# Optimization experiments

Measured on AMD Instinct MI355X. Metric: run time of the kernel, lower is better.

## Reference

```python
import jax, jax.numpy as jnp
import numpy as np

N_NODES = 100000
N_EDGES = 1600000
IN_DIM, HID_DIM, OUT_DIM = 512, 128, 64


def gcn_layer(x, rows, cols, vals, W, b):
    # support = x @ W; out[i] = sum_{e: rows[e]==i} vals[e] * support[cols[e]] + b
    support = x @ W                      # [N, d_out]
    msgs = vals[:, None] * support[cols]  # [E, d_out] gather
    agg = jax.ops.segment_sum(msgs, rows, num_segments=N_NODES)  # scatter-add
    return agg + b


def setup_inputs() -> dict:
    key = jax.random.key(0)
    ks = jax.random.split(key, 8)
    x = jax.random.normal(ks[0], (N_NODES, IN_DIM), dtype=jnp.float32)
    edge_rows = jax.random.randint(ks[1], (N_EDGES,), 0, N_NODES, dtype=jnp.int32)
    edge_cols = jax.random.randint(ks[2], (N_EDGES,), 0, N_NODES, dtype=jnp.int32)
    edge_vals = jax.random.uniform(ks[3], (N_EDGES,), dtype=jnp.float32)
    W0 = jax.random.normal(ks[4], (IN_DIM, HID_DIM), dtype=jnp.float32) / np.sqrt(IN_DIM)
    b0 = jnp.zeros((HID_DIM,), dtype=jnp.float32)
    W1 = jax.random.normal(ks[5], (HID_DIM, OUT_DIM), dtype=jnp.float32) / np.sqrt(HID_DIM)
    b1 = jnp.zeros((OUT_DIM,), dtype=jnp.float32)
    return {"x": x, "edge_rows": edge_rows, "edge_cols": edge_cols,
            "edge_vals": edge_vals, "W0": W0, "b0": b0, "W1": W1, "b1": b1}


def reference(x, edge_rows, edge_cols, edge_vals, W0, b0, W1, b1):
    h = gcn_layer(x, edge_rows, edge_cols, edge_vals, W0, b0)  # GCN0
    h = jax.nn.relu(h)                                          # activation0
    # dropout: identity in eval mode
    out = gcn_layer(h, edge_rows, edge_cols, edge_vals, W1, b1)  # GCN1
    return out
```

## Files before the change

### kernel.cpp

```cpp
#include <hip/hip_runtime.h>

#define N_NODES 100000
#define N_EDGES 1600000
#define NBUCK   ((N_NODES + 127) / 128)
#define BCAP    4096

typedef __attribute__((ext_vector_type(8))) short bf16x8;
typedef __attribute__((ext_vector_type(4))) float f32x4;

__device__ __forceinline__ unsigned short f2bf(float f) {
    unsigned int u = __builtin_bit_cast(unsigned int, f);
    u = (u + 0x7FFFu + ((u >> 16) & 1u)) >> 16;
    return (unsigned short)u;
}
__device__ __forceinline__ float bfu2f(unsigned short u) {
    return __builtin_bit_cast(float, (unsigned int)u << 16);
}
__device__ __forceinline__ uint2 packbf4(float4 v) {
    uint2 p;
    p.x = (unsigned int)f2bf(v.x) | ((unsigned int)f2bf(v.y) << 16);
    p.y = (unsigned int)f2bf(v.z) | ((unsigned int)f2bf(v.w) << 16);
    return p;
}

__device__ __forceinline__ void block_barrier() {
    asm volatile("s_waitcnt lgkmcnt(0)" ::: "memory");
    __builtin_amdgcn_sched_barrier(0);
    __builtin_amdgcn_s_barrier();
    __builtin_amdgcn_sched_barrier(0);
}

__global__ __launch_bounds__(256) void prep_kernel(const float* __restrict__ W0,
                                                   const float* __restrict__ W1,
                                                   unsigned short* __restrict__ W0t,
                                                   unsigned short* __restrict__ W1t,
                                                   int* __restrict__ bcursor) {
    const int i = blockIdx.x * 256 + threadIdx.x;
    if (i < 512 * 128) {
        const int k = i / 128, c = i % 128;
        W0t[c * 512 + k] = f2bf(W0[i]);
    }
    const int j = i - 512 * 128;
    if (j >= 0 && j < 128 * 64) {
        const int k = j / 64, c = j % 64;
        W1t[c * 128 + k] = f2bf(W1[j]);
    }
    const int z = i - (512 * 128 + 128 * 64);
    if (z >= 0 && z < NBUCK) bcursor[z] = z * BCAP;
}

__global__ __launch_bounds__(256) void gemm1_kernel(const float* __restrict__ A,
                                                    const unsigned short* __restrict__ Wt,
                                                    unsigned short* __restrict__ C, int N) {
    constexpr int K   = 512;
    constexpr int M   = 128;
    constexpr int LDT = 40;

    __shared__ __align__(16) unsigned short As[2][64 * LDT];
    __shared__ __align__(16) unsigned short Bs[2][M * LDT];

    const int tid  = threadIdx.x;
    const int lane = tid & 63;
    const int wid  = tid >> 6;
    const int wm   = wid >> 1;
    const int wn   = wid & 1;
    const int brow = blockIdx.x * 64;

    const int ar0 = tid >> 3, akq = tid & 7;
    const int ar1 = ar0 + 32;
    const bool v0 = (brow + ar0) < N;
    const bool v1 = (brow + ar1) < N;
    const float* ap0 = A + (size_t)(brow + ar0) * K + akq * 4;
    const float* ap1 = A + (size_t)(brow + ar1) * K + akq * 4;
    const int br0 = tid >> 2, bkq = tid & 3;
    const unsigned short* bp0 = Wt + (size_t)br0 * K + bkq * 8;
    const unsigned short* bp1 = Wt + (size_t)(br0 + 64) * K + bkq * 8;

    float4 A0a, A0b, A1a, A1b, A2a, A2b, A3a, A3b;
    uint4  B0a, B0b, B1a, B1b, B2a, B2b, B3a, B3b;

#define ISSUE(s, t) do {                                                          \
        const int ko = (t) * 32;                                                  \
        A##s##a = v0 ? *reinterpret_cast<const float4*>(ap0 + ko)                 \
                     : make_float4(0.f, 0.f, 0.f, 0.f);                           \
        A##s##b = v1 ? *reinterpret_cast<const float4*>(ap1 + ko)                 \
                     : make_float4(0.f, 0.f, 0.f, 0.f);                           \
        B##s##a = *reinterpret_cast<const uint4*>(bp0 + ko);                      \
        B##s##b = *reinterpret_cast<const uint4*>(bp1 + ko);                      \
    } while (0)

#define WLDS(s, buf) do {                                                         \
        *reinterpret_cast<uint2*>(&As[buf][ar0 * LDT + akq * 4]) = packbf4(A##s##a); \
        *reinterpret_cast<uint2*>(&As[buf][ar1 * LDT + akq * 4]) = packbf4(A##s##b); \
        *reinterpret_cast<uint4*>(&Bs[buf][br0 * LDT + bkq * 8]) = B##s##a;          \
        *reinterpret_cast<uint4*>(&Bs[buf][(br0 + 64) * LDT + bkq * 8]) = B##s##b;   \
    } while (0)

    f32x4 acc[2][4];
#pragma unroll
    for (int m = 0; m < 2; ++m)
#pragma unroll
        for (int n = 0; n < 4; ++n) acc[m][n] = (f32x4){0.f, 0.f, 0.f, 0.f};

    const int afo = (wm * 32 + (lane & 15)) * LDT + (lane >> 4) * 8;
    const int bfo = (wn * 64 + (lane & 15)) * LDT + (lane >> 4) * 8;

    auto step = [&](int buf) {
        bf16x8 af[2], bfr[4];
#pragma unroll
        for (int m = 0; m < 2; ++m)
            af[m] = *reinterpret_cast<const bf16x8*>(&As[buf][afo + m * 16 * LDT]);
#pragma unroll
        for (int n = 0; n < 4; ++n)
            bfr[n] = *reinterpret_cast<const bf16x8*>(&Bs[buf][bfo + n * 16 * LDT]);
#pragma unroll
        for (int m = 0; m < 2; ++m)
#pragma unroll
            for (int n = 0; n < 4; ++n)
                acc[m][n] = __builtin_amdgcn_mfma_f32_16x16x32_bf16(af[m], bfr[n], acc[m][n], 0, 0, 0);
    };

    ISSUE(0, 0); ISSUE(1, 1); ISSUE(2, 2); ISSUE(3, 3);
    WLDS(0, 0);
    block_barrier();

#pragma unroll
    for (int i = 0; i < 4; ++i) {
        const int t = 4 * i;
        if (t + 4 < 16) ISSUE(0, t + 4);
        step(0);
        WLDS(1, 1);
        block_barrier();
        if (t + 5 < 16) ISSUE(1, t + 5);
        step(1);
        WLDS(2, 0);
        block_barrier();
        if (t + 6 < 16) ISSUE(2, t + 6);
        step(0);
        WLDS(3, 1);
        block_barrier();
        if (t + 7 < 16) ISSUE(3, t + 7);
        step(1);
        if (t + 4 < 16) WLDS(0, 0);
        block_barrier();
    }
#undef ISSUE
#undef WLDS

    const int rb = brow + wm * 32 + ((lane >> 4) * 4);
    const int cb = wn * 64 + (lane & 15);
#pragma unroll
    for (int m = 0; m < 2; ++m)
#pragma unroll
        for (int n = 0; n < 4; ++n)
#pragma unroll
            for (int j = 0; j < 4; ++j) {
                const int r = rb + m * 16 + j;
                if (r < N) C[(size_t)r * M + cb + n * 16] = f2bf(acc[m][n][j]);
            }
}

__global__ __launch_bounds__(256) void gemm2_kernel(const unsigned short* __restrict__ Hb,
                                                    const unsigned short* __restrict__ Wt,
                                                    unsigned short* __restrict__ C) {
    const int gw = (blockIdx.x * 256 + threadIdx.x) >> 6;
    if (gw >= N_NODES / 16) return;
    const int lane = threadIdx.x & 63;
    const int rlo = lane & 15, khi = lane >> 4;
    const int rb = gw * 16;

    const unsigned short* wp = Wt + (size_t)rlo * 128 + khi * 8;
    bf16x8 b[4][4];
#pragma unroll
    for (int n = 0; n < 4; ++n)
#pragma unroll
        for (int t = 0; t < 4; ++t)
            b[n][t] = *reinterpret_cast<const bf16x8*>(wp + (size_t)n * 16 * 128 + t * 32);

    f32x4 acc[4];
#pragma unroll
    for (int n = 0; n < 4; ++n) acc[n] = (f32x4){0.f, 0.f, 0.f, 0.f};

    const unsigned short* hp = Hb + (size_t)(rb + rlo) * 128 + khi * 8;
#pragma unroll
    for (int t = 0; t < 4; ++t) {
        const bf16x8 af = *reinterpret_cast<const bf16x8*>(hp + t * 32);
#pragma unroll
        for (int n = 0; n < 4; ++n)
            acc[n] = __builtin_amdgcn_mfma_f32_16x16x32_bf16(af, b[n][t], acc[n], 0, 0, 0);
    }

#pragma unroll
    for (int n = 0; n < 4; ++n)
#pragma unroll
        for (int j = 0; j < 4; ++j)
            C[(size_t)(rb + khi * 4 + j) * 64 + n * 16 + rlo] = f2bf(acc[n][j]);
}

#define SCAT_CH 4096
__global__ __launch_bounds__(256) void scatter_bucket_kernel(const int* __restrict__ rows,
                                                             const int* __restrict__ cols,
                                                             const float* __restrict__ vals,
                                                             int* __restrict__ bcursor,
                                                             int2* __restrict__ tmp) {
    __shared__ int hist[NBUCK];
    const int tid = threadIdx.x;
    const int e0  = blockIdx.x * SCAT_CH;

    for (int b = tid; b < NBUCK; b += 256) hist[b] = 0;
    __syncthreads();

#pragma unroll
    for (int i = 0; i < SCAT_CH / 256; ++i) {
        const int e = e0 + i * 256 + tid;
        if (e < N_EDGES) atomicAdd(&hist[rows[e] >> 7], 1);
    }
    __syncthreads();

    for (int b = tid; b < NBUCK; b += 256) {
        const int hcnt = hist[b];
        hist[b] = (hcnt > 0) ? atomicAdd(&bcursor[b], hcnt) : 0;
    }
    __syncthreads();

#pragma unroll
    for (int i = 0; i < SCAT_CH / 256; ++i) {
        const int e = e0 + i * 256 + tid;
        if (e < N_EDGES) {
            const int r   = rows[e];
            const int pos = atomicAdd(&hist[r >> 7], 1);
            tmp[pos] = make_int2(cols[e] | ((r & 127) << 17), __float_as_int(vals[e]));
        }
    }
}

__global__ __launch_bounds__(256) void bucket_csr_kernel(const int* __restrict__ bcursor,
                                                         const int2* __restrict__ tmp,
                                                         int2* __restrict__ meta,
                                                         int2* __restrict__ row_range) {
    __shared__ int cnt_sh[128];
    __shared__ int startsh[128];
    __shared__ int cur[128];
    const int b   = blockIdx.x;
    const int tid = threadIdx.x;
    const int base = b * BCAP;
    const int cnt  = bcursor[b] - base;

    if (tid < 128) cnt_sh[tid] = 0;
    __syncthreads();

    for (int j = tid; j < cnt; j += 256)
        atomicAdd(&cnt_sh[((unsigned int)tmp[base + j].x) >> 17], 1);
    __syncthreads();

    if (tid == 0) {
        int a = base;
        for (int i = 0; i < 128; ++i) { startsh[i] = a; a += cnt_sh[i]; }
    }
    __syncthreads();

    if (tid < 128) {
        cur[tid] = startsh[tid];
        const int row = (b << 7) + tid;
        if (row < N_NODES)
            row_range[row] = make_int2(startsh[tid], startsh[tid] + cnt_sh[tid]);
    }
    __syncthreads();

    for (int j = tid; j < cnt; j += 256) {
        const int2 w  = tmp[base + j];
        const int  rl = ((unsigned int)w.x) >> 17;
        const int  pos = atomicAdd(&cur[rl], 1);
        meta[pos] = make_int2(w.x & 0x1FFFF, w.y);
    }
}

template<int DIM, bool RELU_BF16_OUT>
__global__ __launch_bounds__(256) void spmm_kernel(const int2* __restrict__ row_range,
                                                   const int2* __restrict__ meta,
                                                   const unsigned short* __restrict__ sup,
                                                   const float* __restrict__ bias,
                                                   void* __restrict__ aggv) {
    const int wv = (blockIdx.x * 256 + threadIdx.x) >> 6;
    if (wv >= N_NODES) return;
    const int lane = threadIdx.x & 63;

    constexpr int GL = DIM / 8;
    constexpr int NG = 64 / GL;
    constexpr int UN = 2;
    const int grp = lane / GL;
    const int sub = lane % GL;

    const int2 rr = row_range[wv];
    const int start = rr.x, end = rr.y;

    float a[8] = {0.f, 0.f, 0.f, 0.f, 0.f, 0.f, 0.f, 0.f};

    int j = start + grp;
    while (j + (UN - 1) * NG < end) {
        int2 e[UN];
#pragma unroll
        for (int u = 0; u < UN; ++u) e[u] = meta[j + u * NG];
        bf16x8 s[UN];
#pragma unroll
        for (int u = 0; u < UN; ++u)
            s[u] = *reinterpret_cast<const bf16x8*>(sup + (size_t)e[u].x * DIM + sub * 8);
#pragma unroll
        for (int u = 0; u < UN; ++u) {
            const float v = __int_as_float(e[u].y);
#pragma unroll
            for (int d = 0; d < 8; ++d)
                a[d] = fmaf(v, bfu2f((unsigned short)s[u][d]), a[d]);
        }
        j += UN * NG;
    }
    for (; j < end; j += NG) {
        const int2 e = meta[j];
        const bf16x8 s = *reinterpret_cast<const bf16x8*>(sup + (size_t)e.x * DIM + sub * 8);
        const float v = __int_as_float(e.y);
#pragma unroll
        for (int d = 0; d < 8; ++d)
            a[d] = fmaf(v, bfu2f((unsigned short)s[d]), a[d]);
    }

#pragma unroll
    for (int d = 0; d < 8; ++d) {
        if (GL == 8) a[d] += __shfl_xor(a[d], 8);
        a[d] += __shfl_xor(a[d], 16);
        a[d] += __shfl_xor(a[d], 32);
    }

    if (lane < GL) {
        const float4 b0 = *reinterpret_cast<const float4*>(bias + sub * 8);
        const float4 b1 = *reinterpret_cast<const float4*>(bias + sub * 8 + 4);
        float o[8];
        o[0] = a[0] + b0.x; o[1] = a[1] + b0.y; o[2] = a[2] + b0.z; o[3] = a[3] + b0.w;
        o[4] = a[4] + b1.x; o[5] = a[5] + b1.y; o[6] = a[6] + b1.z; o[7] = a[7] + b1.w;
        if (RELU_BF16_OUT) {
            unsigned short* h = (unsigned short*)aggv;
            bf16x8 r;
#pragma unroll
            for (int d = 0; d < 8; ++d) r[d] = (short)f2bf(fmaxf(o[d], 0.f));
            *reinterpret_cast<bf16x8*>(h + (size_t)wv * DIM + sub * 8) = r;
        } else {
            float* og = (float*)aggv;
            float* dst = og + (size_t)wv * DIM + sub * 8;
            *reinterpret_cast<float4*>(dst)     = make_float4(o[0], o[1], o[2], o[3]);
            *reinterpret_cast<float4*>(dst + 4) = make_float4(o[4], o[5], o[6], o[7]);
        }
    }
}

extern "C" void kernel_launch(void* const* d_in, const int* in_sizes, int n_in,
                              void* d_out, int out_size, void* d_ws, size_t ws_size,
                              hipStream_t stream) {
    const float* x    = (const float*)d_in[0];
    const int*   rows = (const int*)d_in[1];
    const int*   cols = (const int*)d_in[2];
    const float* vals = (const float*)d_in[3];
    const float* W0   = (const float*)d_in[4];
    const float* b0   = (const float*)d_in[5];
    const float* W1   = (const float*)d_in[6];
    const float* b1   = (const float*)d_in[7];
    float*       out  = (float*)d_out;

    char* p = (char*)d_ws;
    unsigned short* sup0 = (unsigned short*)p;  p += (size_t)N_NODES * 128 * 2;
    unsigned short* h    = (unsigned short*)p;  p += (size_t)N_NODES * 128 * 2;
    unsigned short* sup1 = (unsigned short*)p;  p += (size_t)N_NODES * 64 * 2;
    unsigned short* W0t  = (unsigned short*)p;  p += (size_t)512 * 128 * 2;
    unsigned short* W1t  = (unsigned short*)p;  p += (size_t)128 * 64 * 2;
    int*   bcursor  = (int*)p;                  p += (size_t)((NBUCK + 3) / 4) * 16;
    int2*  row_range= (int2*)p;                 p += (size_t)N_NODES * 8;
    int2*  tmp      = (int2*)p;                 p += (size_t)NBUCK * BCAP * 8;
    int2*  meta     = (int2*)p;                 p += (size_t)NBUCK * BCAP * 8;

    const int prep_blocks = (512 * 128 + 128 * 64 + NBUCK + 255) / 256;
    const int scat_blocks = (N_EDGES + SCAT_CH - 1) / SCAT_CH;
    const int gemm_blocks = (N_NODES + 63) / 64;
    const int gem2_blocks = (N_NODES / 16 + 3) / 4;
    const int spmm_blocks = (N_NODES * 64 + 255) / 256;

    prep_kernel<<<prep_blocks, 256, 0, stream>>>(W0, W1, W0t, W1t, bcursor);

    scatter_bucket_kernel<<<scat_blocks, 256, 0, stream>>>(rows, cols, vals, bcursor, tmp);
    bucket_csr_kernel<<<NBUCK, 256, 0, stream>>>(bcursor, tmp, meta, row_range);

    gemm1_kernel<<<gemm_blocks, 256, 0, stream>>>(x, W0t, sup0, N_NODES);
    spmm_kernel<128, true><<<spmm_blocks, 256, 0, stream>>>(row_range, meta, sup0, b0, h);

    gemm2_kernel<<<gem2_blocks, 256, 0, stream>>>(h, W1t, sup1);
    spmm_kernel<64, false><<<spmm_blocks, 256, 0, stream>>>(row_range, meta, sup1, b1, out);
}
```

Baseline: 249.0 us.

## Stage gemm1 tiles via direct global-to-LDS loads with fp32 A in LDS

After: 274.8 us. 1.1x slower.

```diff
diff --git a/kernel.cpp b/kernel.cpp
--- a/kernel.cpp
+++ b/kernel.cpp
@@ -16,18 +16,19 @@
 __device__ __forceinline__ float bfu2f(unsigned short u) {
     return __builtin_bit_cast(float, (unsigned int)u << 16);
 }
-__device__ __forceinline__ uint2 packbf4(float4 v) {
-    uint2 p;
-    p.x = (unsigned int)f2bf(v.x) | ((unsigned int)f2bf(v.y) << 16);
-    p.y = (unsigned int)f2bf(v.z) | ((unsigned int)f2bf(v.w) << 16);
-    return p;
-}
-
-__device__ __forceinline__ void block_barrier() {
-    asm volatile("s_waitcnt lgkmcnt(0)" ::: "memory");
-    __builtin_amdgcn_sched_barrier(0);
-    __builtin_amdgcn_s_barrier();
-    __builtin_amdgcn_sched_barrier(0);
+__device__ __forceinline__ bf16x8 pack8(float4 a, float4 b) {
+    bf16x8 r;
+    r[0] = (short)f2bf(a.x); r[1] = (short)f2bf(a.y);
+    r[2] = (short)f2bf(a.z); r[3] = (short)f2bf(a.w);
+    r[4] = (short)f2bf(b.x); r[5] = (short)f2bf(b.y);
+    r[6] = (short)f2bf(b.z); r[7] = (short)f2bf(b.w);
+    return r;
+}
+
+__device__ __forceinline__ void gl_lds16(const void* g, void* s) {
+    __builtin_amdgcn_global_load_lds(
+        (const __attribute__((address_space(1))) void*)g,
+        (__attribute__((address_space(3))) void*)s, 16, 0, 0);
 }
 
 __global__ __launch_bounds__(256) void prep_kernel(const float* __restrict__ W0,
@@ -52,49 +53,28 @@
 __global__ __launch_bounds__(256) void gemm1_kernel(const float* __restrict__ A,
                                                     const unsigned short* __restrict__ Wt,
                                                     unsigned short* __restrict__ C, int N) {
-    constexpr int K   = 512;
-    constexpr int M   = 128;
-    constexpr int LDT = 40;
-
-    __shared__ __align__(16) unsigned short As[2][64 * LDT];
-    __shared__ __align__(16) unsigned short Bs[2][M * LDT];
+    __shared__ __align__(16) float4 AsF4[2][8 * 64];
+    __shared__ __align__(16) uint4  Bs4[2][4 * 128];
 
     const int tid  = threadIdx.x;
     const int lane = tid & 63;
-    const int wid  = tid >> 6;
-    const int wm   = wid >> 1;
-    const int wn   = wid & 1;
+    const int w    = tid >> 6;
+    const int wm   = w >> 1;
+    const int wn   = w & 1;
     const int brow = blockIdx.x * 64;
 
-    const int ar0 = tid >> 3, akq = tid & 7;
-    const int ar1 = ar0 + 32;
-    const bool v0 = (brow + ar0) < N;
-    const bool v1 = (brow + ar1) < N;
-    const float* ap0 = A + (size_t)(brow + ar0) * K + akq * 4;
-    const float* ap1 = A + (size_t)(brow + ar1) * K + akq * 4;
-    const int br0 = tid >> 2, bkq = tid & 3;
-    const unsigned short* bp0 = Wt + (size_t)br0 * K + bkq * 8;
-    const unsigned short* bp1 = Wt + (size_t)(br0 + 64) * K + bkq * 8;
-
-    float4 A0a, A0b, A1a, A1b, A2a, A2b, A3a, A3b;
-    uint4  B0a, B0b, B1a, B1b, B2a, B2b, B3a, B3b;
-
-#define ISSUE(s, t) do {                                                          \
-        const int ko = (t) * 32;                                                  \
-        A##s##a = v0 ? *reinterpret_cast<const float4*>(ap0 + ko)                 \
-                     : make_float4(0.f, 0.f, 0.f, 0.f);                           \
-        A##s##b = v1 ? *reinterpret_cast<const float4*>(ap1 + ko)                 \
-                     : make_float4(0.f, 0.f, 0.f, 0.f);                           \
-        B##s##a = *reinterpret_cast<const uint4*>(bp0 + ko);                      \
-        B##s##b = *reinterpret_cast<const uint4*>(bp1 + ko);                      \
-    } while (0)
-
-#define WLDS(s, buf) do {                                                         \
-        *reinterpret_cast<uint2*>(&As[buf][ar0 * LDT + akq * 4]) = packbf4(A##s##a); \
-        *reinterpret_cast<uint2*>(&As[buf][ar1 * LDT + akq * 4]) = packbf4(A##s##b); \
-        *reinterpret_cast<uint4*>(&Bs[buf][br0 * LDT + bkq * 8]) = B##s##a;          \
-        *reinterpret_cast<uint4*>(&Bs[buf][(br0 + 64) * LDT + bkq * 8]) = B##s##b;   \
-    } while (0)
+    const int grow = min(brow + lane, N - 1);
+    const float* asrc = A + (size_t)grow * 512;
+    const unsigned short* bsrc0 = Wt + (size_t)(lane)      * 512 + w * 8;
+    const unsigned short* bsrc1 = Wt + (size_t)(64 + lane) * 512 + w * 8;
+
+    auto stage = [&](int t, int buf) {
+        const int koA = t * 32;
+        gl_lds16(asrc + koA + (2 * w)     * 4, &AsF4[buf][(2 * w)     * 64]);
+        gl_lds16(asrc + koA + (2 * w + 1) * 4, &AsF4[buf][(2 * w + 1) * 64]);
+        gl_lds16(bsrc0 + t * 32,               &Bs4[buf][(2 * w)     * 64]);
+        gl_lds16(bsrc1 + t * 32,               &Bs4[buf][(2 * w + 1) * 64]);
+    };
 
     f32x4 acc[2][4];
 #pragma unroll
@@ -102,17 +82,25 @@
 #pragma unroll
         for (int n = 0; n < 4; ++n) acc[m][n] = (f32x4){0.f, 0.f, 0.f, 0.f};
 
-    const int afo = (wm * 32 + (lane & 15)) * LDT + (lane >> 4) * 8;
-    const int bfo = (wn * 64 + (lane & 15)) * LDT + (lane >> 4) * 8;
+    const int kq  = lane >> 4;
+    const int rlo = lane & 15;
 
     auto step = [&](int buf) {
-        bf16x8 af[2], bfr[4];
-#pragma unroll
-        for (int m = 0; m < 2; ++m)
-            af[m] = *reinterpret_cast<const bf16x8*>(&As[buf][afo + m * 16 * LDT]);
-#pragma unroll
-        for (int n = 0; n < 4; ++n)
-            bfr[n] = *reinterpret_cast<const bf16x8*>(&Bs[buf][bfo + n * 16 * LDT]);
+        bf16x8 af[2];
+#pragma unroll
+        for (int m = 0; m < 2; ++m) {
+            const int row = wm * 32 + m * 16 + rlo;
+            const float4 lo = AsF4[buf][(kq * 2 + 0) * 64 + row];
+            const float4 hi = AsF4[buf][(kq * 2 + 1) * 64 + row];
+            af[m] = pack8(lo, hi);
+        }
+        bf16x8 bfr[4];
+#pragma unroll
+        for (int n = 0; n < 4; ++n) {
+            const int col = wn * 64 + n * 16 + rlo;
+            const uint4 u = Bs4[buf][kq * 128 + col];
+            bfr[n] = __builtin_bit_cast(bf16x8, u);
+        }
 #pragma unroll
         for (int m = 0; m < 2; ++m)
 #pragma unroll
@@ -120,35 +108,18 @@
                 acc[m][n] = __builtin_amdgcn_mfma_f32_16x16x32_bf16(af[m], bfr[n], acc[m][n], 0, 0, 0);
     };
 
-    ISSUE(0, 0); ISSUE(1, 1); ISSUE(2, 2); ISSUE(3, 3);
-    WLDS(0, 0);
-    block_barrier();
-
-#pragma unroll
-    for (int i = 0; i < 4; ++i) {
-        const int t = 4 * i;
-        if (t + 4 < 16) ISSUE(0, t + 4);
-        step(0);
-        WLDS(1, 1);
-        block_barrier();
-        if (t + 5 < 16) ISSUE(1, t + 5);
-        step(1);
-        WLDS(2, 0);
-        block_barrier();
-        if (t + 6 < 16) ISSUE(2, t + 6);
-        step(0);
-        WLDS(3, 1);
-        block_barrier();
-        if (t + 7 < 16) ISSUE(3, t + 7);
-        step(1);
-        if (t + 4 < 16) WLDS(0, 0);
-        block_barrier();
-    }
-#undef ISSUE
-#undef WLDS
-
-    const int rb = brow + wm * 32 + ((lane >> 4) * 4);
-    const int cb = wn * 64 + (lane & 15);
+    stage(0, 0);
+    __syncthreads();
+
+#pragma unroll
+    for (int t = 0; t < 16; ++t) {
+        if (t + 1 < 16) stage(t + 1, (t + 1) & 1);
+        step(t & 1);
+        __syncthreads();
+    }
+
+    const int rb = brow + wm * 32 + kq * 4;
+    const int cb = wn * 64 + rlo;
 #pragma unroll
     for (int m = 0; m < 2; ++m)
 #pragma unroll
@@ -156,7 +127,7 @@
 #pragma unroll
             for (int j = 0; j < 4; ++j) {
                 const int r = rb + m * 16 + j;
-                if (r < N) C[(size_t)r * M + cb + n * 16] = f2bf(acc[m][n][j]);
+                if (r < N) C[(size_t)r * 128 + cb + n * 16] = f2bf(acc[m][n][j]);
             }
 }
 
```
